# Performance work log

Hardware: AMD Instinct MI355X
Metric: run time of the kernel (lower is better)

Reference implementation:

```python
import jax, jax.numpy as jnp
import numpy as np

B, CIN, COUT, H, W = 16, 64, 64, 128, 128
KH, KW = 3, 3
PAD, STRIDE = 1, 1


def setup_inputs() -> dict:
    key = jax.random.key(0)
    k1, k2 = jax.random.split(key)
    x = jax.random.normal(k1, (B, CIN, H, W), dtype=jnp.float32)
    scale = (1.0 / (CIN * KH * KW)) ** 0.5
    weight = jax.random.normal(k2, (COUT, CIN, KH, KW), dtype=jnp.float32) * scale
    bias = jnp.zeros((COUT,), dtype=jnp.float32)
    return {"x": x, "weight": weight, "bias": bias}


def reference(x, weight, bias):
    # Faithful translation of FFTConv2d.forward (including its einsum semantics:
    # 'bchw,oihw->bohw' sums over c and i independently, as in the torch source).
    b, c, h, w = x.shape
    kh, kw = weight.shape[2], weight.shape[3]
    pad_h = h + kh - 1  # 130
    pad_w = w + kw - 1  # 130
    x_padded = jnp.pad(x, ((0, 0), (0, 0), (0, pad_h - h), (0, pad_w - w)))
    w_padded = jnp.pad(weight, ((0, 0), (0, 0), (0, pad_h - kh), (0, pad_w - kw)))
    X_fft = jnp.fft.rfft2(x_padded)                  # [B,C,pad_h,pad_w//2+1]
    W_fft = jnp.fft.rfft2(w_padded, s=(pad_h, pad_w))  # [O,I,pad_h,pad_w//2+1]
    Y_fft = jnp.einsum('bchw,oihw->bohw', X_fft, W_fft)
    y = jnp.fft.irfft2(Y_fft, s=(pad_h, pad_w))      # [B,O,pad_h,pad_w]
    # torch: y[:, :, padding:-padding or None:stride, padding:-padding or None:stride]
    y = y[:, :, PAD:-PAD:STRIDE, PAD:-PAD:STRIDE]    # [B,O,H,W] for PAD=1,STRIDE=1
    y = y + bias[None, :, None, None]
    return y
```

## Files before the change

kernel.cpp:

```cpp
#include <hip/hip_runtime.h>

typedef float f32x4 __attribute__((ext_vector_type(4)));

#define NB 16
#define NC 64
#define NH 128
#define NW 128

#define PROWS 130
#define PCOLS 136
#define XVOL  (NB * PROWS * PCOLS)
#define WOFF  XVOL

__global__ void prep_kernel(const float* __restrict__ wgt, float* __restrict__ ws) {
  int gid = blockIdx.x * 256 + threadIdx.x;
  if (gid < XVOL / 4) {
    ((f32x4*)ws)[gid] = (f32x4){0.f, 0.f, 0.f, 0.f};
  }
  if (gid < 64 * 9) {
    int o = gid / 9;
    int t = gid - o * 9;
    int r = t / 3;
    int s = t - r * 3;
    const float* wp = wgt + o * (NC * 9) + (2 - r) * 3 + (2 - s);
    float acc = 0.f;
    #pragma unroll
    for (int i = 0; i < NC; ++i) acc += wp[i * 9];
    ws[WOFF + o * 9 + t] = acc;
  }
}

__global__ __launch_bounds__(256) void reduce_kernel(const float* __restrict__ x,
                                                     float* __restrict__ ws) {
  int idx = blockIdx.x * 256 + threadIdx.x;
  int b   = idx >> 12;
  int rem = idx & 4095;
  int p   = rem >> 5;
  int q0  = (rem & 31) << 2;

  const float* xp = x + b * (NC * NH * NW) + p * NW + q0;
  f32x4 acc = {0.f, 0.f, 0.f, 0.f};
  #pragma unroll 8
  for (int c = 0; c < NC; ++c) {
    f32x4 v = *(const f32x4*)(xp + c * (NH * NW));
    acc += v;
  }
  *(f32x4*)&ws[(b * PROWS + p + 1) * PCOLS + 4 + q0] = acc;
}

__global__ __launch_bounds__(256) void conv_kernel(const float* __restrict__ ws,
                                                   const float* __restrict__ bias,
                                                   float* __restrict__ out) {
  int bid = blockIdx.x;
  int b   = bid >> 9;
  int o   = (bid >> 3) & 63;
  int blk = bid & 7;

  int t     = threadIdx.x;
  int row16 = t >> 4;
  int cg    = t & 15;
  int p     = blk * 16 + row16;
  int q0    = cg * 8;

  const float* wf = ws + WOFF + o * 9;
  float w0 = wf[0], w1 = wf[1], w2 = wf[2];
  float w3 = wf[3], w4 = wf[4], w5 = wf[5];
  float w6 = wf[6], w7 = wf[7], w8 = wf[8];
  float bb = bias[o];

  const float* xp = ws + (b * PROWS + p) * PCOLS + (q0 + 3);
  float r0[10], r1[10], r2[10];
  #pragma unroll
  for (int j = 0; j < 10; ++j) {
    r0[j] = xp[j];
    r1[j] = xp[PCOLS + j];
    r2[j] = xp[2 * PCOLS + j];
  }

  float y[8];
  #pragma unroll
  for (int j = 0; j < 8; ++j) {
    float acc = bb;
    acc += w0 * r0[j] + w1 * r0[j + 1] + w2 * r0[j + 2];
    acc += w3 * r1[j] + w4 * r1[j + 1] + w5 * r1[j + 2];
    acc += w6 * r2[j] + w7 * r2[j + 1] + w8 * r2[j + 2];
    y[j] = acc;
  }

  float* op = out + ((b * 64 + o) * NH + p) * NW + q0;
  *(f32x4*)op       = (f32x4){y[0], y[1], y[2], y[3]};
  *(f32x4*)(op + 4) = (f32x4){y[4], y[5], y[6], y[7]};
}

extern "C" void kernel_launch(void* const* d_in, const int* in_sizes, int n_in,
                              void* d_out, int out_size, void* d_ws, size_t ws_size,
                              hipStream_t stream) {
  const float* x    = (const float*)d_in[0];
  const float* wgt  = (const float*)d_in[1];
  const float* bias = (const float*)d_in[2];
  float* out = (float*)d_out;
  float* ws  = (float*)d_ws;
  (void)in_sizes; (void)n_in; (void)out_size; (void)ws_size;

  prep_kernel<<<dim3((XVOL / 4 + 255) / 256), dim3(256), 0, stream>>>(wgt, ws);
  reduce_kernel<<<dim3(NB * NH * NW / 4 / 256), dim3(256), 0, stream>>>(x, ws);
  conv_kernel<<<dim3(NB * 64 * 8), dim3(256), 0, stream>>>(ws, bias, out);
}
```

Before: 137.6 us.

## Fuse prep and channel-reduce kernels, zero only halo, vectorize conv loads

Merges the weight-sum prep kernel and the channel-sum reduce kernel into one launch. Extra blocks compute the weight tap sums cooperatively through shared memory and zero only the padding halo, instead of clearing the whole workspace. The conv kernel now loads its input rows as aligned float4 vectors rather than scalars, and the reduce loop uses two accumulators. This removes a kernel launch and a full workspace memset pass, at the cost of a single weight block that may become a slow tail.

```diff
diff --git a/kernel.cpp b/kernel.cpp
--- a/kernel.cpp
+++ b/kernel.cpp
@@ -11,41 +11,68 @@
 #define PCOLS 136
 #define XVOL  (NB * PROWS * PCOLS)
 #define WOFF  XVOL
+#define NRED  (NB * NH * NW / 4 / 256)
 
-__global__ void prep_kernel(const float* __restrict__ wgt, float* __restrict__ ws) {
-  int gid = blockIdx.x * 256 + threadIdx.x;
-  if (gid < XVOL / 4) {
-    ((f32x4*)ws)[gid] = (f32x4){0.f, 0.f, 0.f, 0.f};
+__global__ __launch_bounds__(256) void reduce_prep_kernel(
+    const float* __restrict__ x, const float* __restrict__ wgt,
+    float* __restrict__ ws) {
+  __shared__ float red[64][9][4];
+
+  const int bid = blockIdx.x;
+  const int t   = threadIdx.x;
+
+  if (bid < NRED) {
+    int idx = bid * 256 + t;
+    int b   = idx >> 12;
+    int rem = idx & 4095;
+    int p   = rem >> 5;
+    int q0  = (rem & 31) << 2;
+
+    const float* xp = x + b * (NC * NH * NW) + p * NW + q0;
+    f32x4 acc0 = {0.f, 0.f, 0.f, 0.f};
+    f32x4 acc1 = {0.f, 0.f, 0.f, 0.f};
+    #pragma unroll 8
+    for (int c = 0; c < NC; c += 2) {
+      acc0 += *(const f32x4*)(xp + c * (NH * NW));
+      acc1 += *(const f32x4*)(xp + (c + 1) * (NH * NW));
+    }
+    f32x4 acc = acc0 + acc1;
+    *(f32x4*)&ws[(b * PROWS + p + 1) * PCOLS + 4 + q0] = acc;
+  } else if (bid == NRED) {
+    int quarter = t & 3;
+    int o       = t >> 2;
+    const float* base = wgt + o * (NC * 9) + quarter * (16 * 9);
+    float part[9] = {0.f, 0.f, 0.f, 0.f, 0.f, 0.f, 0.f, 0.f, 0.f};
+    #pragma unroll
+    for (int i = 0; i < 16; ++i) {
+      #pragma unroll
+      for (int t9 = 0; t9 < 9; ++t9) part[t9] += base[i * 9 + t9];
+    }
+    #pragma unroll
+    for (int t9 = 0; t9 < 9; ++t9) red[o][t9][quarter] = part[t9];
+    __syncthreads();
+    for (int s = t; s < 64 * 9; s += 256) {
+      int o2 = s / 9;
+      int t9 = s - o2 * 9;
+      float v = red[o2][t9][0] + red[o2][t9][1] + red[o2][t9][2] + red[o2][t9][3];
+      ws[WOFF + o2 * 9 + (8 - t9)] = v;
+    }
+  } else {
+    for (int idx = t; idx < NB * 2 * PCOLS; idx += 256) {
+      int b   = idx / (2 * PCOLS);
+      int rem = idx - b * (2 * PCOLS);
+      int rr  = (rem >= PCOLS) ? (PROWS - 1) : 0;
+      int col = (rem >= PCOLS) ? (rem - PCOLS) : rem;
+      ws[(b * PROWS + rr) * PCOLS + col] = 0.f;
+    }
+    for (int idx = t; idx < NB * NH * 2; idx += 256) {
+      int b   = idx >> 8;
+      int rem = idx & 255;
+      int row = 1 + (rem >> 1);
+      int col = (rem & 1) ? 132 : 3;
+      ws[(b * PROWS + row) * PCOLS + col] = 0.f;
+    }
   }
-  if (gid < 64 * 9) {
-    int o = gid / 9;
-    int t = gid - o * 9;
-    int r = t / 3;
-    int s = t - r * 3;
-    const float* wp = wgt + o * (NC * 9) + (2 - r) * 3 + (2 - s);
-    float acc = 0.f;
-    #pragma unroll
-    for (int i = 0; i < NC; ++i) acc += wp[i * 9];
-    ws[WOFF + o * 9 + t] = acc;
-  }
-}
-
-__global__ __launch_bounds__(256) void reduce_kernel(const float* __restrict__ x,
-                                                     float* __restrict__ ws) {
-  int idx = blockIdx.x * 256 + threadIdx.x;
-  int b   = idx >> 12;
-  int rem = idx & 4095;
-  int p   = rem >> 5;
-  int q0  = (rem & 31) << 2;
-
-  const float* xp = x + b * (NC * NH * NW) + p * NW + q0;
-  f32x4 acc = {0.f, 0.f, 0.f, 0.f};
-  #pragma unroll 8
-  for (int c = 0; c < NC; ++c) {
-    f32x4 v = *(const f32x4*)(xp + c * (NH * NW));
-    acc += v;
-  }
-  *(f32x4*)&ws[(b * PROWS + p + 1) * PCOLS + 4 + q0] = acc;
 }
 
 __global__ __launch_bounds__(256) void conv_kernel(const float* __restrict__ ws,
@@ -68,24 +95,30 @@
   float w6 = wf[6], w7 = wf[7], w8 = wf[8];
   float bb = bias[o];
 
-  const float* xp = ws + (b * PROWS + p) * PCOLS + (q0 + 3);
-  float r0[10], r1[10], r2[10];
+  const float* bp = ws + (b * PROWS + p) * PCOLS + q0;
+  f32x4 L0[4], L1[4], L2[4];
   #pragma unroll
-  for (int j = 0; j < 10; ++j) {
-    r0[j] = xp[j];
-    r1[j] = xp[PCOLS + j];
-    r2[j] = xp[2 * PCOLS + j];
+  for (int k = 0; k < 4; ++k) {
+    L0[k] = *(const f32x4*)(bp + 4 * k);
+    L1[k] = *(const f32x4*)(bp + PCOLS + 4 * k);
+    L2[k] = *(const f32x4*)(bp + 2 * PCOLS + 4 * k);
   }
 
+#define E0(j) (L0[(j) >> 2][(j) & 3])
+#define E1(j) (L1[(j) >> 2][(j) & 3])
+#define E2(j) (L2[(j) >> 2][(j) & 3])
   float y[8];
   #pragma unroll
   for (int j = 0; j < 8; ++j) {
     float acc = bb;
-    acc += w0 * r0[j] + w1 * r0[j + 1] + w2 * r0[j + 2];
-    acc += w3 * r1[j] + w4 * r1[j + 1] + w5 * r1[j + 2];
-    acc += w6 * r2[j] + w7 * r2[j + 1] + w8 * r2[j + 2];
+    acc += w0 * E0(j + 3) + w1 * E0(j + 4) + w2 * E0(j + 5);
+    acc += w3 * E1(j + 3) + w4 * E1(j + 4) + w5 * E1(j + 5);
+    acc += w6 * E2(j + 3) + w7 * E2(j + 4) + w8 * E2(j + 5);
     y[j] = acc;
   }
+#undef E0
+#undef E1
+#undef E2
 
   float* op = out + ((b * 64 + o) * NH + p) * NW + q0;
   *(f32x4*)op       = (f32x4){y[0], y[1], y[2], y[3]};
@@ -102,7 +135,6 @@
   float* ws  = (float*)d_ws;
   (void)in_sizes; (void)n_in; (void)out_size; (void)ws_size;
 
-  prep_kernel<<<dim3((XVOL / 4 + 255) / 256), dim3(256), 0, stream>>>(wgt, ws);
-  reduce_kernel<<<dim3(NB * NH * NW / 4 / 256), dim3(256), 0, stream>>>(x, ws);
+  reduce_prep_kernel<<<dim3(NRED + 2), dim3(256), 0, stream>>>(x, wgt, ws);
   conv_kernel<<<dim3(NB * 64 * 8), dim3(256), 0, stream>>>(ws, bias, out);
 }
```

Result: faster. 131.2 us (-4.7%).

## Fuse channel reduction, weight collapse and 3x3 conv into one kernel

Applied to the files above, without the earlier changes.

Replaces the three launches (workspace zeroing plus weight sum, channel reduction, conv) with one kernel per (batch, 8-row stripe). Each block sums the 64 input channels for its 10 halo rows into LDS, recomputes the channel-summed and flipped 3x3 weights, then writes all 64 output channels from register-held inputs. This drops the workspace round trip and two launches. In exchange, about 25% of input rows are re-read for halos, every block redundantly reduces the weights, and only 256 blocks are launched, which may leave the GPU underfilled.

```diff
diff --git a/kernel.cpp b/kernel.cpp
--- a/kernel.cpp
+++ b/kernel.cpp
@@ -6,90 +6,109 @@
 #define NC 64
 #define NH 128
 #define NW 128
+#define STRIPE 8
+#define LROWS (STRIPE + 2)
+#define LCOLS 136
 
-#define PROWS 130
-#define PCOLS 136
-#define XVOL  (NB * PROWS * PCOLS)
-#define WOFF  XVOL
+__global__ __launch_bounds__(256) void fused_conv_kernel(
+    const float* __restrict__ x, const float* __restrict__ wgt,
+    const float* __restrict__ bias, float* __restrict__ out) {
+  __shared__ float xs[LROWS][LCOLS];
+  __shared__ float red[64][9][4];
+  __shared__ float wl[64][12];
 
-__global__ void prep_kernel(const float* __restrict__ wgt, float* __restrict__ ws) {
-  int gid = blockIdx.x * 256 + threadIdx.x;
-  if (gid < XVOL / 4) {
-    ((f32x4*)ws)[gid] = (f32x4){0.f, 0.f, 0.f, 0.f};
-  }
-  if (gid < 64 * 9) {
-    int o = gid / 9;
-    int t = gid - o * 9;
-    int r = t / 3;
-    int s = t - r * 3;
-    const float* wp = wgt + o * (NC * 9) + (2 - r) * 3 + (2 - s);
-    float acc = 0.f;
-    #pragma unroll
-    for (int i = 0; i < NC; ++i) acc += wp[i * 9];
-    ws[WOFF + o * 9 + t] = acc;
-  }
-}
+  const int t   = threadIdx.x;
+  const int bid = blockIdx.x;
+  const int b   = bid >> 4;
+  const int R0  = (bid & 15) * STRIPE;
 
-__global__ __launch_bounds__(256) void reduce_kernel(const float* __restrict__ x,
-                                                     float* __restrict__ ws) {
-  int idx = blockIdx.x * 256 + threadIdx.x;
-  int b   = idx >> 12;
-  int rem = idx & 4095;
-  int p   = rem >> 5;
-  int q0  = (rem & 31) << 2;
+  {
+    const int lr = t >> 5;
+    const int g  = t & 31;
+    const int ir = R0 - 1 + lr;
+    f32x4 a0 = {0,0,0,0}, a1 = {0,0,0,0}, a2 = {0,0,0,0}, a3 = {0,0,0,0};
+    if (ir >= 0 && ir < NH) {
+      const float* xp = x + (b * NC * NH + ir) * NW + g * 4;
+      #pragma unroll 4
+      for (int c = 0; c < NC; c += 4) {
+        a0 += *(const f32x4*)(xp + (c + 0) * (NH * NW));
+        a1 += *(const f32x4*)(xp + (c + 1) * (NH * NW));
+        a2 += *(const f32x4*)(xp + (c + 2) * (NH * NW));
+        a3 += *(const f32x4*)(xp + (c + 3) * (NH * NW));
+      }
+    }
+    *(f32x4*)&xs[lr][4 + g * 4] = (a0 + a1) + (a2 + a3);
 
-  const float* xp = x + b * (NC * NH * NW) + p * NW + q0;
-  f32x4 acc = {0.f, 0.f, 0.f, 0.f};
-  #pragma unroll 8
-  for (int c = 0; c < NC; ++c) {
-    f32x4 v = *(const f32x4*)(xp + c * (NH * NW));
-    acc += v;
-  }
-  *(f32x4*)&ws[(b * PROWS + p + 1) * PCOLS + 4 + q0] = acc;
-}
-
-__global__ __launch_bounds__(256) void conv_kernel(const float* __restrict__ ws,
-                                                   const float* __restrict__ bias,
-                                                   float* __restrict__ out) {
-  int bid = blockIdx.x;
-  int b   = bid >> 9;
-  int o   = (bid >> 3) & 63;
-  int blk = bid & 7;
-
-  int t     = threadIdx.x;
-  int row16 = t >> 4;
-  int cg    = t & 15;
-  int p     = blk * 16 + row16;
-  int q0    = cg * 8;
-
-  const float* wf = ws + WOFF + o * 9;
-  float w0 = wf[0], w1 = wf[1], w2 = wf[2];
-  float w3 = wf[3], w4 = wf[4], w5 = wf[5];
-  float w6 = wf[6], w7 = wf[7], w8 = wf[8];
-  float bb = bias[o];
-
-  const float* xp = ws + (b * PROWS + p) * PCOLS + (q0 + 3);
-  float r0[10], r1[10], r2[10];
-  #pragma unroll
-  for (int j = 0; j < 10; ++j) {
-    r0[j] = xp[j];
-    r1[j] = xp[PCOLS + j];
-    r2[j] = xp[2 * PCOLS + j];
+    if (t < 64) {
+      const int lr2 = 8 + (t >> 5);
+      const int ir2 = R0 - 1 + lr2;
+      f32x4 c0 = {0,0,0,0}, c1 = {0,0,0,0}, c2 = {0,0,0,0}, c3 = {0,0,0,0};
+      if (ir2 >= 0 && ir2 < NH) {
+        const float* xp = x + (b * NC * NH + ir2) * NW + g * 4;
+        #pragma unroll 4
+        for (int c = 0; c < NC; c += 4) {
+          c0 += *(const f32x4*)(xp + (c + 0) * (NH * NW));
+          c1 += *(const f32x4*)(xp + (c + 1) * (NH * NW));
+          c2 += *(const f32x4*)(xp + (c + 2) * (NH * NW));
+          c3 += *(const f32x4*)(xp + (c + 3) * (NH * NW));
+        }
+      }
+      *(f32x4*)&xs[lr2][4 + g * 4] = (c0 + c1) + (c2 + c3);
+    }
+    if (t < 2 * LROWS) xs[t >> 1][(t & 1) ? 132 : 3] = 0.f;
   }
 
-  float y[8];
-  #pragma unroll
-  for (int j = 0; j < 8; ++j) {
-    float acc = bb;
-    acc += w0 * r0[j] + w1 * r0[j + 1] + w2 * r0[j + 2];
-    acc += w3 * r1[j] + w4 * r1[j + 1] + w5 * r1[j + 2];
-    acc += w6 * r2[j] + w7 * r2[j + 1] + w8 * r2[j + 2];
-    y[j] = acc;
+  {
+    const int o  = t >> 2;
+    const int qr = t & 3;
+    const float* wp = wgt + o * (NC * 9) + qr * (16 * 9);
+    float part[9] = {0.f, 0.f, 0.f, 0.f, 0.f, 0.f, 0.f, 0.f, 0.f};
+    #pragma unroll
+    for (int i = 0; i < 16; ++i) {
+      #pragma unroll
+      for (int k = 0; k < 9; ++k) part[k] += wp[i * 9 + k];
+    }
+    #pragma unroll
+    for (int k = 0; k < 9; ++k) red[o][k][qr] = part[k];
   }
+  __syncthreads();
 
-  float* op = out + ((b * 64 + o) * NH + p) * NW + q0;
-  *(f32x4*)op       = (f32x4){y[0], y[1], y[2], y[3]};
-  *(f32x4*)(op + 4) = (f32x4){y[4], y[5], y[6], y[7]};
+  for (int s2 = t; s2 < 576; s2 += 256) {
+    int o  = s2 / 9;
+    int t9 = s2 - o * 9;
+    wl[o][8 - t9] = red[o][t9][0] + red[o][t9][1] + red[o][t9][2] + red[o][t9][3];
+  }
+  if (t < 64) wl[t][9] = bias[t];
+  __syncthreads();
+
+  {
+    const int ro = t >> 5;
+    const int g  = t & 31;
+    const int q0 = g * 4;
+    float X0[6], X1[6], X2[6];
+    #pragma unroll
+    for (int m = 0; m < 6; ++m) {
+      X0[m] = xs[ro][q0 + 3 + m];
+      X1[m] = xs[ro + 1][q0 + 3 + m];
+      X2[m] = xs[ro + 2][q0 + 3 + m];
+    }
+    float* op = out + ((b * 64) * NH + R0 + ro) * NW + q0;
+    for (int o = 0; o < 64; ++o) {
+      f32x4 wa = *(const f32x4*)&wl[o][0];
+      f32x4 wb = *(const f32x4*)&wl[o][4];
+      f32x4 wc = *(const f32x4*)&wl[o][8];
+      f32x4 y;
+      #pragma unroll
+      for (int jj = 0; jj < 4; ++jj) {
+        float acc = wc[1];
+        acc += wa[0] * X0[jj] + wa[1] * X0[jj + 1] + wa[2] * X0[jj + 2];
+        acc += wa[3] * X1[jj] + wb[0] * X1[jj + 1] + wb[1] * X1[jj + 2];
+        acc += wb[2] * X2[jj] + wb[3] * X2[jj + 1] + wc[0] * X2[jj + 2];
+        y[jj] = acc;
+      }
+      *(f32x4*)(op + o * (NH * NW)) = y;
+    }
+  }
 }
 
 extern "C" void kernel_launch(void* const* d_in, const int* in_sizes, int n_in,
@@ -99,10 +118,7 @@
   const float* wgt  = (const float*)d_in[1];
   const float* bias = (const float*)d_in[2];
   float* out = (float*)d_out;
-  float* ws  = (float*)d_ws;
-  (void)in_sizes; (void)n_in; (void)out_size; (void)ws_size;
+  (void)in_sizes; (void)n_in; (void)out_size; (void)d_ws; (void)ws_size;
 
-  prep_kernel<<<dim3((XVOL / 4 + 255) / 256), dim3(256), 0, stream>>>(wgt, ws);
-  reduce_kernel<<<dim3(NB * NH * NW / 4 / 256), dim3(256), 0, stream>>>(x, ws);
-  conv_kernel<<<dim3(NB * 64 * 8), dim3(256), 0, stream>>>(ws, bias, out);
+  fused_conv_kernel<<<dim3(NB * (NH / STRIPE)), dim3(256), 0, stream>>>(x, wgt, bias, out);
 }
```

After: 120.1 us. 1.15x faster.
